# Kernel optimization log

Hardware: AMD Instinct MI355X
Metric: run time of the kernel (lower is better)

## Reference

```python
import jax, jax.numpy as jnp
import numpy as np

B, TT, TP, TO = 8, 128, 256, 512
V, D, H, L = 1024, 1024, 16, 12
FF = 4 * D
DH = D // H
EPS = 1e-5


def _pe(t, d):
    # sinusoidal PE: concat(sin(omega*t), cos(omega*t)), omega = exp(-ln(1e4)*i/(d/2))
    half = d // 2
    omega = jnp.exp(-jnp.log(10000.0) * jnp.arange(half, dtype=jnp.float32) / half)
    ang = jnp.arange(t, dtype=jnp.float32)[:, None] * omega[None, :]  # (t, d/2)
    return jnp.concatenate([jnp.sin(ang), jnp.cos(ang)], axis=-1)  # (t, d)


def _ln(x, g, b):
    mu = x.mean(axis=-1, keepdims=True)
    var = ((x - mu) ** 2).mean(axis=-1, keepdims=True)
    return (x - mu) / jnp.sqrt(var + EPS) * g + b


def _forward(text_ids, prompt_ids, output_ids, text_tab, prompt_tab, output_tab, sep,
             ln1_g, ln1_b, qkv_w, out_w, out_b, ln2_g, ln2_b,
             ff1_w, ff1_b, ff2_w, ff2_b, fc_w, fc_b):
    emb = lambda ids, tab: tab[ids] + _pe(ids.shape[1], D)[None]
    sep_tok = jnp.broadcast_to(sep, (B, 1, D))
    # join: [text, sep, prompt, sep, output]
    x = jnp.concatenate([emb(text_ids, text_tab), sep_tok,
                         emb(prompt_ids, prompt_tab), sep_tok,
                         emb(output_ids, output_tab)], axis=1)  # (B, T, D)
    T = x.shape[1]
    causal = jnp.tril(jnp.ones((T, T), dtype=bool))  # (T, T)
    scale = DH ** -0.5
    neg = -jnp.finfo(x.dtype).max
    for l in range(L):
        # attention block (prenorm residual); uniform lengths -> mask m is all ones
        h = _ln(x, ln1_g[l], ln1_b[l])
        qkv = h @ qkv_w[l]  # (B, T, 3D)
        q, k, v = jnp.split(qkv, 3, axis=-1)
        q = q.reshape(B, T, H, DH)
        k = k.reshape(B, T, H, DH)
        v = v.reshape(B, T, H, DH)
        e = jnp.einsum('bihd,bjhd->bijh', q, k) * scale
        e = jnp.where(causal[None, :, :, None], e, neg)
        a = jax.nn.softmax(e, axis=2)
        o = jnp.einsum('bijh,bjhd->bihd', a, v).reshape(B, T, D)
        x = x + o @ out_w[l] + out_b[l]
        # ffn block (prenorm residual), exact GELU as torch nn.GELU default
        h2 = _ln(x, ln2_g[l], ln2_b[l])
        ff = jax.nn.gelu(h2 @ ff1_w[l] + ff1_b[l], approximate=False) @ ff2_w[l] + ff2_b[l]
        x = x + ff
    h = x @ fc_w + fc_b  # (B, T, V)
    return h[:, -1, :]  # logits of last position, (B, V)


def setup_inputs() -> dict:
    key = jax.random.key(0)
    ks = iter(jax.random.split(key, 32))
    s = 0.02
    inp = {
        'text_ids': jax.random.randint(next(ks), (B, TT), 0, V),
        'prompt_ids': jax.random.randint(next(ks), (B, TP), 0, V),
        'output_ids': jax.random.randint(next(ks), (B, TO), 0, V),
        'text_tab': jax.random.normal(next(ks), (V, D), jnp.float32) * s,
        'prompt_tab': jax.random.normal(next(ks), (V, D), jnp.float32) * s,
        'output_tab': jax.random.normal(next(ks), (V, D), jnp.float32) * s,
        'sep': jax.random.normal(next(ks), (D,), jnp.float32),
        'ln1_g': jnp.ones((L, D), jnp.float32),
        'ln1_b': jnp.zeros((L, D), jnp.float32),
        'qkv_w': jax.random.normal(next(ks), (L, D, 3 * D), jnp.float32) * s,
        'out_w': jax.random.normal(next(ks), (L, D, D), jnp.float32) * s,
        'out_b': jnp.zeros((L, D), jnp.float32),
        'ln2_g': jnp.ones((L, D), jnp.float32),
        'ln2_b': jnp.zeros((L, D), jnp.float32),
        'ff1_w': jax.random.normal(next(ks), (L, D, FF), jnp.float32) * s,
        'ff1_b': jnp.zeros((L, FF), jnp.float32),
        'ff2_w': jax.random.normal(next(ks), (L, FF, D), jnp.float32) * s,
        'ff2_b': jnp.zeros((L, D), jnp.float32),
        'fc_w': jax.random.normal(next(ks), (D, V), jnp.float32) * s,
        'fc_b': jnp.zeros((V,), jnp.float32),
    }
    return inp


def reference(text_ids, prompt_ids, output_ids, text_tab, prompt_tab, output_tab, sep,
              ln1_g, ln1_b, qkv_w, out_w, out_b, ln2_g, ln2_b,
              ff1_w, ff1_b, ff2_w, ff2_b, fc_w, fc_b):
    return _forward(text_ids, prompt_ids, output_ids, text_tab, prompt_tab, output_tab, sep,
                    ln1_g, ln1_b, qkv_w, out_w, out_b, ln2_g, ln2_b,
                    ff1_w, ff1_b, ff2_w, ff2_b, fc_w, fc_b)
```

## Files before the change

### kernel.cpp

```cpp
#include <hip/hip_runtime.h>
#include <hip/hip_bf16.h>
#include <math.h>

#define Bn 8
#define Tn 898
#define Dn 1024
#define Hn 16
#define DHn 64
#define Ln 12
#define FFn 4096
#define Vn 1024
#define BT (Bn*Tn)

typedef short bf16x8 __attribute__((ext_vector_type(8)));
typedef float f32x4 __attribute__((ext_vector_type(4)));

__device__ __forceinline__ ushort f2bf(float f) {
    union { float f; unsigned u; } c; c.f = f;
    unsigned r = c.u + 0x7fffu + ((c.u >> 16) & 1u);
    return (ushort)(r >> 16);
}

__device__ __forceinline__ void glds16(const void* g, void* l) {
    __builtin_amdgcn_global_load_lds(
        (const __attribute__((address_space(1))) unsigned int*)g,
        (__attribute__((address_space(3))) unsigned int*)l, 16, 0, 0);
}

__global__ __launch_bounds__(256) void transpose_cast_kernel(
    const float* __restrict__ in, ushort* __restrict__ out,
    int K, int N, size_t in_ls, size_t out_ls)
{
    __shared__ ushort t[64][68];
    const float* inp = in + (size_t)blockIdx.z * in_ls;
    ushort* outp = out + (size_t)blockIdx.z * out_ls;
    int n0 = blockIdx.x * 64, k0 = blockIdx.y * 64;
    int tx = threadIdx.x & 63, ty = threadIdx.x >> 6;
    #pragma unroll
    for (int p = 0; p < 16; p++) {
        int kl = p * 4 + ty;
        t[tx][kl] = f2bf(inp[(size_t)(k0 + kl) * N + n0 + tx]);
    }
    __syncthreads();
    int tx4 = threadIdx.x & 15, ty4 = threadIdx.x >> 4;
    #pragma unroll
    for (int p = 0; p < 4; p++) {
        int nl = p * 16 + ty4;
        ushort4 v;
        v.x = t[nl][4*tx4]; v.y = t[nl][4*tx4+1]; v.z = t[nl][4*tx4+2]; v.w = t[nl][4*tx4+3];
        *(ushort4*)&outp[(size_t)(n0 + nl) * K + k0 + 4*tx4] = v;
    }
}

__global__ __launch_bounds__(256) void embed_kernel(
    const int* __restrict__ tids, const int* __restrict__ pids, const int* __restrict__ oids,
    const float* __restrict__ ttab, const float* __restrict__ ptab, const float* __restrict__ otab,
    const float* __restrict__ sep, float* __restrict__ x)
{
    int bp = blockIdx.x;
    int b = bp / Tn, pos = bp - b * Tn;
    int d0 = threadIdx.x * 4;
    float4 r;
    if (pos == 128 || pos == 385) {
        r = *(const float4*)(sep + d0);
    } else {
        int t; int id; const float* tab;
        if (pos < 128)      { t = pos;       id = tids[b*128 + t]; tab = ttab; }
        else if (pos < 385) { t = pos - 129; id = pids[b*256 + t]; tab = ptab; }
        else                { t = pos - 386; id = oids[b*512 + t]; tab = otab; }
        float4 e = *(const float4*)(tab + (size_t)id * Dn + d0);
        float pe[4];
        #pragma unroll
        for (int i = 0; i < 4; i++) {
            int d = d0 + i;
            int ii = d & 511;
            float omega = expf(-9.210340371976184f * (float)ii * (1.0f/512.0f));
            float ang = (float)t * omega;
            pe[i] = (d < 512) ? sinf(ang) : cosf(ang);
        }
        r.x = e.x + pe[0]; r.y = e.y + pe[1]; r.z = e.z + pe[2]; r.w = e.w + pe[3];
    }
    *(float4*)(x + (size_t)bp * Dn + d0) = r;
}

__global__ __launch_bounds__(256) void ln_kernel(
    const float* __restrict__ x, const float* __restrict__ g, const float* __restrict__ bt,
    ushort* __restrict__ out)
{
    __shared__ float red[8];
    int row = blockIdx.x, tid = threadIdx.x;
    float4 v = ((const float4*)(x + (size_t)row * Dn))[tid];
    float s = v.x + v.y + v.z + v.w;
    #pragma unroll
    for (int o = 32; o; o >>= 1) s += __shfl_down(s, o);
    if ((tid & 63) == 0) red[tid >> 6] = s;
    __syncthreads();
    float mu = (red[0] + red[1] + red[2] + red[3]) * (1.0f / Dn);
    float d0 = v.x - mu, d1 = v.y - mu, d2 = v.z - mu, d3 = v.w - mu;
    float s2 = d0*d0 + d1*d1 + d2*d2 + d3*d3;
    #pragma unroll
    for (int o = 32; o; o >>= 1) s2 += __shfl_down(s2, o);
    if ((tid & 63) == 0) red[4 + (tid >> 6)] = s2;
    __syncthreads();
    float var = (red[4] + red[5] + red[6] + red[7]) * (1.0f / Dn);
    float rstd = rsqrtf(var + 1e-5f);
    float4 gg = ((const float4*)g)[tid];
    float4 bb = ((const float4*)bt)[tid];
    ushort4 o4;
    o4.x = f2bf(d0 * rstd * gg.x + bb.x);
    o4.y = f2bf(d1 * rstd * gg.y + bb.y);
    o4.z = f2bf(d2 * rstd * gg.z + bb.z);
    o4.w = f2bf(d3 * rstd * gg.w + bb.w);
    ((ushort4*)(out + (size_t)row * Dn))[tid] = o4;
}

template<int MODE>
__global__ __launch_bounds__(256) void gemm_kernel(
    const ushort* __restrict__ A, const ushort* __restrict__ Bw,
    const float* __restrict__ bias, const float* __restrict__ resid,
    void* __restrict__ Cout, int M, int N, int K)
{
    __shared__ ushort Asm[128 * 32];
    __shared__ ushort Bsm[128 * 32];
    int tid = threadIdx.x;
    int lane = tid & 63, wv = tid >> 6;
    int wm = wv >> 1, wn = wv & 1;
    int m0 = blockIdx.y * 128, n0 = blockIdx.x * 128;
    int l16 = lane & 15, lhi = lane >> 4;

    f32x4 acc[4][4];
    #pragma unroll
    for (int i = 0; i < 4; i++)
        #pragma unroll
        for (int j = 0; j < 4; j++) acc[i][j] = (f32x4){0.f, 0.f, 0.f, 0.f};

    int srow = wv * 16 + (lane >> 2);
    int skc  = (lane & 3) * 8;
    const ushort* Ap0 = A  + (size_t)(m0 + srow) * K + skc;
    const ushort* Ap1 = A  + (size_t)(m0 + 64 + srow) * K + skc;
    const ushort* Bp0 = Bw + (size_t)(n0 + srow) * K + skc;
    const ushort* Bp1 = Bw + (size_t)(n0 + 64 + srow) * K + skc;
    ushort* ldsA0 = &Asm[wv * 512];
    ushort* ldsA1 = &Asm[2048 + wv * 512];
    ushort* ldsB0 = &Bsm[wv * 512];
    ushort* ldsB1 = &Bsm[2048 + wv * 512];

    for (int kk = 0; kk < K; kk += 32) {
        __syncthreads();
        glds16(Ap0 + kk, ldsA0);
        glds16(Ap1 + kk, ldsA1);
        glds16(Bp0 + kk, ldsB0);
        glds16(Bp1 + kk, ldsB1);
        __syncthreads();

        bf16x8 af[4], bfr[4];
        #pragma unroll
        for (int mi = 0; mi < 4; mi++)
            af[mi] = *(const bf16x8*)&Asm[(wm*64 + mi*16 + l16) * 32 + lhi*8];
        #pragma unroll
        for (int ni = 0; ni < 4; ni++)
            bfr[ni] = *(const bf16x8*)&Bsm[(wn*64 + ni*16 + l16) * 32 + lhi*8];
        #pragma unroll
        for (int mi = 0; mi < 4; mi++)
            #pragma unroll
            for (int ni = 0; ni < 4; ni++)
                acc[mi][ni] = __builtin_amdgcn_mfma_f32_16x16x32_bf16(af[mi], bfr[ni], acc[mi][ni], 0, 0, 0);
    }

    #pragma unroll
    for (int mi = 0; mi < 4; mi++) {
        int rl = wm*64 + mi*16 + lhi*4;
        #pragma unroll
        for (int ni = 0; ni < 4; ni++) {
            int gcol = n0 + wn*64 + ni*16 + l16;
            float bs = (MODE == 0) ? 0.0f : bias[gcol];
            #pragma unroll
            for (int j = 0; j < 4; j++) {
                int grow = m0 + rl + j;
                if (grow >= M) continue;
                float v = acc[mi][ni][j] + bs;
                if (MODE == 1) {
                    float r = resid[(size_t)grow * N + gcol];
                    ((float*)Cout)[(size_t)grow * N + gcol] = r + v;
                } else if (MODE == 2) {
                    v = 0.5f * v * (1.0f + erff(v * 0.70710678118654752f));
                    ((ushort*)Cout)[(size_t)grow * N + gcol] = f2bf(v);
                } else {
                    ((ushort*)Cout)[(size_t)grow * N + gcol] = f2bf(v);
                }
            }
        }
    }
}

__global__ __launch_bounds__(256) void attn_kernel(
    const ushort* __restrict__ qkv, ushort* __restrict__ out)
{
    __shared__ ushort Ksm[64 * 72];
    __shared__ ushort Vsm[64 * 72];
    __shared__ ushort Psm[4][16 * 72];
    int qt = blockIdx.x, b = blockIdx.y, h = blockIdx.z;
    int tid = threadIdx.x, lane = tid & 63, wave = tid >> 6;
    int l16 = lane & 15, lhi = lane >> 4;

    int qrow = qt*64 + wave*16 + l16;
    bf16x8 qf0 = {}, qf1 = {};
    if (qrow < Tn) {
        const ushort* qp = qkv + (size_t)(b*Tn + qrow) * 3072 + h*64 + lhi*8;
        qf0 = *(const bf16x8*)qp;
        qf1 = *(const bf16x8*)(qp + 32);
    }

    f32x4 o[4];
    #pragma unroll
    for (int i = 0; i < 4; i++) o[i] = (f32x4){0.f,0.f,0.f,0.f};
    float mrun[4] = {-1e30f,-1e30f,-1e30f,-1e30f};
    float sume[4] = {0.f,0.f,0.f,0.f};

    int kr = tid >> 2, cc = (tid & 3) * 16;
    const ushort* kvbase = qkv + (size_t)(b*Tn) * 3072 + h*64 + cc;
    int qg = qt*64 + wave*16 + lhi*4;

    for (int jt = 0; jt <= qt; jt++) {
        int kvr = jt*64 + kr;
        uint4 k0 = make_uint4(0,0,0,0), k1 = k0, v0 = k0, v1 = k0;
        if (kvr < Tn) {
            const ushort* p = kvbase + (size_t)kvr * 3072;
            k0 = *(const uint4*)(p + 1024);
            k1 = *(const uint4*)(p + 1024 + 8);
            v0 = *(const uint4*)(p + 2048);
            v1 = *(const uint4*)(p + 2048 + 8);
        }
        __syncthreads();
        *(uint4*)&Ksm[kr * 72 + cc] = k0;
        *(uint4*)&Ksm[kr * 72 + cc + 8] = k1;
        {
            ushort vv[16];
            *(uint4*)&vv[0] = v0; *(uint4*)&vv[8] = v1;
            #pragma unroll
            for (int i = 0; i < 16; i++) Vsm[(cc + i) * 72 + kr] = vv[i];
        }
        __syncthreads();

        f32x4 s[4];
        #pragma unroll
        for (int ni = 0; ni < 4; ni++) {
            s[ni] = (f32x4){0.f,0.f,0.f,0.f};
            bf16x8 kf0 = *(const bf16x8*)&Ksm[(ni*16 + l16) * 72 + lhi*8];
            bf16x8 kf1 = *(const bf16x8*)&Ksm[(ni*16 + l16) * 72 + lhi*8 + 32];
            s[ni] = __builtin_amdgcn_mfma_f32_16x16x32_bf16(qf0, kf0, s[ni], 0, 0, 0);
            s[ni] = __builtin_amdgcn_mfma_f32_16x16x32_bf16(qf1, kf1, s[ni], 0, 0, 0);
        }

        float pv[4][4];
        #pragma unroll
        for (int j = 0; j < 4; j++) {
            int qgj = qg + j;
            float mx = -1e30f;
            #pragma unroll
            for (int ni = 0; ni < 4; ni++) {
                int kvg = jt*64 + ni*16 + l16;
                float e = (kvg <= qgj && kvg < Tn) ? s[ni][j] * 0.125f : -1e30f;
                pv[ni][j] = e;
                mx = fmaxf(mx, e);
            }
            #pragma unroll
            for (int m = 1; m < 16; m <<= 1) mx = fmaxf(mx, __shfl_xor(mx, m));
            float mnew = fmaxf(mrun[j], mx);
            float fac = expf(mrun[j] - mnew);
            mrun[j] = mnew;
            float rs = 0.f;
            #pragma unroll
            for (int ni = 0; ni < 4; ni++) { pv[ni][j] = expf(pv[ni][j] - mnew); rs += pv[ni][j]; }
            #pragma unroll
            for (int m = 1; m < 16; m <<= 1) rs += __shfl_xor(rs, m);
            sume[j] = sume[j] * fac + rs;
            #pragma unroll
            for (int di = 0; di < 4; di++) o[di][j] *= fac;
        }

        #pragma unroll
        for (int j = 0; j < 4; j++)
            #pragma unroll
            for (int ni = 0; ni < 4; ni++)
                Psm[wave][(lhi*4 + j) * 72 + ni*16 + l16] = f2bf(pv[ni][j]);
        __syncthreads();

        bf16x8 pf0 = *(const bf16x8*)&Psm[wave][l16 * 72 + lhi*8];
        bf16x8 pf1 = *(const bf16x8*)&Psm[wave][l16 * 72 + lhi*8 + 32];
        #pragma unroll
        for (int di = 0; di < 4; di++) {
            bf16x8 vf0 = *(const bf16x8*)&Vsm[(di*16 + l16) * 72 + lhi*8];
            bf16x8 vf1 = *(const bf16x8*)&Vsm[(di*16 + l16) * 72 + lhi*8 + 32];
            o[di] = __builtin_amdgcn_mfma_f32_16x16x32_bf16(pf0, vf0, o[di], 0, 0, 0);
            o[di] = __builtin_amdgcn_mfma_f32_16x16x32_bf16(pf1, vf1, o[di], 0, 0, 0);
        }
    }

    #pragma unroll
    for (int j = 0; j < 4; j++) {
        int qgj = qg + j;
        if (qgj >= Tn) continue;
        float inv = 1.0f / sume[j];
        #pragma unroll
        for (int di = 0; di < 4; di++)
            out[(size_t)(b*Tn + qgj) * Dn + h*64 + di*16 + l16] = f2bf(o[di][j] * inv);
    }
}

__global__ __launch_bounds__(256) void fc_kernel(
    const float* __restrict__ x, const float* __restrict__ w,
    const float* __restrict__ bias, float* __restrict__ out)
{
    __shared__ float xs[Dn];
    int b = blockIdx.y;
    int v = blockIdx.x * 256 + threadIdx.x;
    float4 t = ((const float4*)(x + (size_t)(b*Tn + Tn - 1) * Dn))[threadIdx.x];
    ((float4*)xs)[threadIdx.x] = t;
    __syncthreads();
    float acc = bias[v];
    for (int d = 0; d < Dn; d++)
        acc = fmaf(xs[d], w[(size_t)d * Vn + v], acc);
    out[(size_t)b * Vn + v] = acc;
}

extern "C" void kernel_launch(void* const* d_in, const int* in_sizes, int n_in,
                              void* d_out, int out_size, void* d_ws, size_t ws_size,
                              hipStream_t stream)
{
    const int*   text_ids  = (const int*)d_in[0];
    const int*   prompt_ids= (const int*)d_in[1];
    const int*   output_ids= (const int*)d_in[2];
    const float* text_tab  = (const float*)d_in[3];
    const float* prompt_tab= (const float*)d_in[4];
    const float* output_tab= (const float*)d_in[5];
    const float* sep       = (const float*)d_in[6];
    const float* ln1_g     = (const float*)d_in[7];
    const float* ln1_b     = (const float*)d_in[8];
    const float* qkv_w     = (const float*)d_in[9];
    const float* out_w     = (const float*)d_in[10];
    const float* out_b     = (const float*)d_in[11];
    const float* ln2_g     = (const float*)d_in[12];
    const float* ln2_b     = (const float*)d_in[13];
    const float* ff1_w     = (const float*)d_in[14];
    const float* ff1_b     = (const float*)d_in[15];
    const float* ff2_w     = (const float*)d_in[16];
    const float* ff2_b     = (const float*)d_in[17];
    const float* fc_w      = (const float*)d_in[18];
    const float* fc_b      = (const float*)d_in[19];

    char* ws = (char*)d_ws;
    float*  x    = (float*)(ws);
    ushort* h    = (ushort*)(ws + 29425664);
    ushort* qkv  = (ushort*)(ws + 44138496);
    ushort* attn = (ushort*)(ws + 88276992);
    ushort* ff1o = (ushort*)(ws + 102989824);
    ushort* wT   = (ushort*)(ws + 161841152);

    const size_t L_STRIDE = 12582912;
    const size_t OFF_QKV = 0, OFF_OUT = 3145728, OFF_FF1 = 4194304, OFF_FF2 = 8388608;
    const size_t upfront_need = 161841152ULL + 2ULL * L_STRIDE * Ln;
    const bool upfront = ws_size >= upfront_need;
    const int ZL = upfront ? Ln : 1;

    if (upfront) {
        transpose_cast_kernel<<<dim3(48,16,Ln), 256, 0, stream>>>(qkv_w, wT + OFF_QKV, Dn, 3*Dn, (size_t)Dn*3*Dn, L_STRIDE);
        transpose_cast_kernel<<<dim3(16,16,Ln), 256, 0, stream>>>(out_w, wT + OFF_OUT, Dn, Dn,   (size_t)Dn*Dn,   L_STRIDE);
        transpose_cast_kernel<<<dim3(64,16,Ln), 256, 0, stream>>>(ff1_w, wT + OFF_FF1, Dn, FFn,  (size_t)Dn*FFn,  L_STRIDE);
        transpose_cast_kernel<<<dim3(16,64,Ln), 256, 0, stream>>>(ff2_w, wT + OFF_FF2, FFn, Dn,  (size_t)FFn*Dn,  L_STRIDE);
    }

    embed_kernel<<<BT, 256, 0, stream>>>(text_ids, prompt_ids, output_ids,
                                         text_tab, prompt_tab, output_tab, sep, x);

    const int MT = 57;
    for (int l = 0; l < Ln; l++) {
        ushort* wbase = upfront ? (wT + (size_t)l * L_STRIDE) : wT;
        if (!upfront) {
            transpose_cast_kernel<<<dim3(48,16,1), 256, 0, stream>>>(qkv_w + (size_t)l*Dn*3*Dn, wbase + OFF_QKV, Dn, 3*Dn, 0, 0);
            transpose_cast_kernel<<<dim3(16,16,1), 256, 0, stream>>>(out_w + (size_t)l*Dn*Dn,   wbase + OFF_OUT, Dn, Dn,   0, 0);
            transpose_cast_kernel<<<dim3(64,16,1), 256, 0, stream>>>(ff1_w + (size_t)l*Dn*FFn,  wbase + OFF_FF1, Dn, FFn,  0, 0);
            transpose_cast_kernel<<<dim3(16,64,1), 256, 0, stream>>>(ff2_w + (size_t)l*FFn*Dn,  wbase + OFF_FF2, FFn, Dn,  0, 0);
        }
        ln_kernel<<<BT, 256, 0, stream>>>(x, ln1_g + l*Dn, ln1_b + l*Dn, h);
        gemm_kernel<0><<<dim3(3*Dn/128, MT), 256, 0, stream>>>(
            h, wbase + OFF_QKV, nullptr, nullptr, qkv, BT, 3*Dn, Dn);
        attn_kernel<<<dim3(15, Bn, Hn), 256, 0, stream>>>(qkv, attn);
        gemm_kernel<1><<<dim3(Dn/128, MT), 256, 0, stream>>>(
            attn, wbase + OFF_OUT, out_b + l*Dn, x, x, BT, Dn, Dn);
        ln_kernel<<<BT, 256, 0, stream>>>(x, ln2_g + l*Dn, ln2_b + l*Dn, h);
        gemm_kernel<2><<<dim3(FFn/128, MT), 256, 0, stream>>>(
            h, wbase + OFF_FF1, ff1_b + l*FFn, nullptr, ff1o, BT, FFn, Dn);
        gemm_kernel<1><<<dim3(Dn/128, MT), 256, 0, stream>>>(
            ff1o, wbase + OFF_FF2, ff2_b + l*Dn, x, x, BT, Dn, FFn);
    }

    fc_kernel<<<dim3(Vn/256, Bn), 256, 0, stream>>>(x, fc_w, fc_b, (float*)d_out);
}
```

Before: 5.908 ms.

## Rewrite GEMM with templated tiles, double-buffered LDS, and XCD-aware block mapping

Replaces the fixed 128x128, K=32 GEMM with a templated kernel. The kernel double-buffers 64-wide K tiles in LDS, so loads for the next tile overlap the current tile's MFMAs, and it needs one barrier per step instead of two. QKV and FF1 use 256x256 tiles with 8 waves, while out-proj and FF2 keep 128x128. Blocks are remapped so contiguous tiles land on the same XCD to improve L2 reuse. Workspace offsets grow to cover the padded M of 29x256 rows, since A loads past row 7184 now read into the enlarged buffers.

```diff
diff --git a/kernel.cpp b/kernel.cpp
--- a/kernel.cpp
+++ b/kernel.cpp
@@ -11,6 +11,7 @@
 #define FFn 4096
 #define Vn 1024
 #define BT (Bn*Tn)
+#define MP 7424
 
 typedef short bf16x8 __attribute__((ext_vector_type(8)));
 typedef float f32x4 __attribute__((ext_vector_type(4)));
@@ -114,65 +115,91 @@
     ((ushort4*)(out + (size_t)row * Dn))[tid] = o4;
 }
 
-template<int MODE>
-__global__ __launch_bounds__(256) void gemm_kernel(
+template<int BM, int BN, int WM, int WN, int MODE>
+__global__ __launch_bounds__(WM*WN*64) void gemm2_kernel(
     const ushort* __restrict__ A, const ushort* __restrict__ Bw,
     const float* __restrict__ bias, const float* __restrict__ resid,
-    void* __restrict__ Cout, int M, int N, int K)
-{
-    __shared__ ushort Asm[128 * 32];
-    __shared__ ushort Bsm[128 * 32];
-    int tid = threadIdx.x;
-    int lane = tid & 63, wv = tid >> 6;
-    int wm = wv >> 1, wn = wv & 1;
-    int m0 = blockIdx.y * 128, n0 = blockIdx.x * 128;
+    void* __restrict__ Cout, int M, int N, int K, int nx)
+{
+    constexpr int NWAVE = WM * WN;
+    constexpr int MI = BM / WM / 16;
+    constexpr int NI = BN / WN / 16;
+    constexpr int GA = (BM / 8) / NWAVE;
+    constexpr int GB = (BN / 8) / NWAVE;
+
+    __shared__ ushort sA[2][BM * 64];
+    __shared__ ushort sB[2][BN * 64];
+
+    int tid = threadIdx.x, lane = tid & 63, wv = tid >> 6;
+    int wm = wv / WN, wn = wv % WN;
     int l16 = lane & 15, lhi = lane >> 4;
 
-    f32x4 acc[4][4];
-    #pragma unroll
-    for (int i = 0; i < 4; i++)
-        #pragma unroll
-        for (int j = 0; j < 4; j++) acc[i][j] = (f32x4){0.f, 0.f, 0.f, 0.f};
-
-    int srow = wv * 16 + (lane >> 2);
-    int skc  = (lane & 3) * 8;
-    const ushort* Ap0 = A  + (size_t)(m0 + srow) * K + skc;
-    const ushort* Ap1 = A  + (size_t)(m0 + 64 + srow) * K + skc;
-    const ushort* Bp0 = Bw + (size_t)(n0 + srow) * K + skc;
-    const ushort* Bp1 = Bw + (size_t)(n0 + 64 + srow) * K + skc;
-    ushort* ldsA0 = &Asm[wv * 512];
-    ushort* ldsA1 = &Asm[2048 + wv * 512];
-    ushort* ldsB0 = &Bsm[wv * 512];
-    ushort* ldsB1 = &Bsm[2048 + wv * 512];
-
-    for (int kk = 0; kk < K; kk += 32) {
+    int nb = gridDim.x, bid = blockIdx.x;
+    int q = nb >> 3, r = nb & 7;
+    int xcd = bid & 7, idx = bid >> 3;
+    int wg = (xcd < r ? xcd * (q + 1) : r * (q + 1) + (xcd - r) * q) + idx;
+    int mt = wg / nx, ntt = wg - mt * nx;
+    int m0 = mt * BM, n0 = ntt * BN;
+
+    f32x4 acc[MI][NI];
+    #pragma unroll
+    for (int i = 0; i < MI; i++)
+        #pragma unroll
+        for (int j = 0; j < NI; j++) acc[i][j] = (f32x4){0.f, 0.f, 0.f, 0.f};
+
+    const int sr = lane >> 3;
+    const int sc = (lane & 7) * 8;
+    const ushort* Ab = A + (size_t)m0 * K + sc;
+    const ushort* Bb = Bw + (size_t)n0 * K + sc;
+
+    auto STAGE = [&](int buf, int kk) {
+        #pragma unroll
+        for (int i = 0; i < GA; i++) {
+            int rg = wv * GA + i;
+            glds16(Ab + (size_t)(rg * 8 + sr) * K + kk, &sA[buf][rg * 512]);
+        }
+        #pragma unroll
+        for (int i = 0; i < GB; i++) {
+            int rg = wv * GB + i;
+            glds16(Bb + (size_t)(rg * 8 + sr) * K + kk, &sB[buf][rg * 512]);
+        }
+    };
+
+    auto COMPUTE = [&](int buf) {
+        #pragma unroll
+        for (int ks = 0; ks < 2; ks++) {
+            bf16x8 af[MI], bfr[NI];
+            #pragma unroll
+            for (int mi = 0; mi < MI; mi++)
+                af[mi] = *(const bf16x8*)&sA[buf][(wm * (16 * MI) + mi * 16 + l16) * 64 + ks * 32 + lhi * 8];
+            #pragma unroll
+            for (int ni = 0; ni < NI; ni++)
+                bfr[ni] = *(const bf16x8*)&sB[buf][(wn * (16 * NI) + ni * 16 + l16) * 64 + ks * 32 + lhi * 8];
+            #pragma unroll
+            for (int mi = 0; mi < MI; mi++)
+                #pragma unroll
+                for (int ni = 0; ni < NI; ni++)
+                    acc[mi][ni] = __builtin_amdgcn_mfma_f32_16x16x32_bf16(af[mi], bfr[ni], acc[mi][ni], 0, 0, 0);
+        }
+    };
+
+    int ntile = K >> 6;
+    STAGE(0, 0);
+    __syncthreads();
+    int cur = 0;
+    for (int t = 0; t < ntile; t++) {
+        if (t + 1 < ntile) STAGE(cur ^ 1, (t + 1) * 64);
+        COMPUTE(cur);
         __syncthreads();
-        glds16(Ap0 + kk, ldsA0);
-        glds16(Ap1 + kk, ldsA1);
-        glds16(Bp0 + kk, ldsB0);
-        glds16(Bp1 + kk, ldsB1);
-        __syncthreads();
-
-        bf16x8 af[4], bfr[4];
-        #pragma unroll
-        for (int mi = 0; mi < 4; mi++)
-            af[mi] = *(const bf16x8*)&Asm[(wm*64 + mi*16 + l16) * 32 + lhi*8];
-        #pragma unroll
-        for (int ni = 0; ni < 4; ni++)
-            bfr[ni] = *(const bf16x8*)&Bsm[(wn*64 + ni*16 + l16) * 32 + lhi*8];
-        #pragma unroll
-        for (int mi = 0; mi < 4; mi++)
-            #pragma unroll
-            for (int ni = 0; ni < 4; ni++)
-                acc[mi][ni] = __builtin_amdgcn_mfma_f32_16x16x32_bf16(af[mi], bfr[ni], acc[mi][ni], 0, 0, 0);
-    }
-
-    #pragma unroll
-    for (int mi = 0; mi < 4; mi++) {
-        int rl = wm*64 + mi*16 + lhi*4;
-        #pragma unroll
-        for (int ni = 0; ni < 4; ni++) {
-            int gcol = n0 + wn*64 + ni*16 + l16;
+        cur ^= 1;
+    }
+
+    #pragma unroll
+    for (int mi = 0; mi < MI; mi++) {
+        int rl = wm * (16 * MI) + mi * 16 + lhi * 4;
+        #pragma unroll
+        for (int ni = 0; ni < NI; ni++) {
+            int gcol = n0 + wn * (16 * NI) + ni * 16 + l16;
             float bs = (MODE == 0) ? 0.0f : bias[gcol];
             #pragma unroll
             for (int j = 0; j < 4; j++) {
@@ -180,8 +207,8 @@
                 if (grow >= M) continue;
                 float v = acc[mi][ni][j] + bs;
                 if (MODE == 1) {
-                    float r = resid[(size_t)grow * N + gcol];
-                    ((float*)Cout)[(size_t)grow * N + gcol] = r + v;
+                    float rr = resid[(size_t)grow * N + gcol];
+                    ((float*)Cout)[(size_t)grow * N + gcol] = rr + v;
                 } else if (MODE == 2) {
                     v = 0.5f * v * (1.0f + erff(v * 0.70710678118654752f));
                     ((ushort*)Cout)[(size_t)grow * N + gcol] = f2bf(v);
@@ -352,16 +379,15 @@
     char* ws = (char*)d_ws;
     float*  x    = (float*)(ws);
     ushort* h    = (ushort*)(ws + 29425664);
-    ushort* qkv  = (ushort*)(ws + 44138496);
-    ushort* attn = (ushort*)(ws + 88276992);
-    ushort* ff1o = (ushort*)(ws + 102989824);
-    ushort* wT   = (ushort*)(ws + 161841152);
+    ushort* qkv  = (ushort*)(ws + 44630016);
+    ushort* attn = (ushort*)(ws + 90243072);
+    ushort* ff1o = (ushort*)(ws + 105447424);
+    ushort* wT   = (ushort*)(ws + 166264832);
 
     const size_t L_STRIDE = 12582912;
     const size_t OFF_QKV = 0, OFF_OUT = 3145728, OFF_FF1 = 4194304, OFF_FF2 = 8388608;
-    const size_t upfront_need = 161841152ULL + 2ULL * L_STRIDE * Ln;
+    const size_t upfront_need = 166264832ULL + 2ULL * L_STRIDE * Ln;
     const bool upfront = ws_size >= upfront_need;
-    const int ZL = upfront ? Ln : 1;
 
     if (upfront) {
         transpose_cast_kernel<<<dim3(48,16,Ln), 256, 0, stream>>>(qkv_w, wT + OFF_QKV, Dn, 3*Dn, (size_t)Dn*3*Dn, L_STRIDE);
@@ -373,26 +399,25 @@
     embed_kernel<<<BT, 256, 0, stream>>>(text_ids, prompt_ids, output_ids,
                                          text_tab, prompt_tab, output_tab, sep, x);
 
-    const int MT = 57;
     for (int l = 0; l < Ln; l++) {
-        ushort* wbase = upfront ? (wT + (size_t)l * L_STRIDE) : wT;
+        ushort* wb = upfront ? (wT + (size_t)l * L_STRIDE) : wT;
         if (!upfront) {
-            transpose_cast_kernel<<<dim3(48,16,1), 256, 0, stream>>>(qkv_w + (size_t)l*Dn*3*Dn, wbase + OFF_QKV, Dn, 3*Dn, 0, 0);
-            transpose_cast_kernel<<<dim3(16,16,1), 256, 0, stream>>>(out_w + (size_t)l*Dn*Dn,   wbase + OFF_OUT, Dn, Dn,   0, 0);
-            transpose_cast_kernel<<<dim3(64,16,1), 256, 0, stream>>>(ff1_w + (size_t)l*Dn*FFn,  wbase + OFF_FF1, Dn, FFn,  0, 0);
-            transpose_cast_kernel<<<dim3(16,64,1), 256, 0, stream>>>(ff2_w + (size_t)l*FFn*Dn,  wbase + OFF_FF2, FFn, Dn,  0, 0);
+            transpose_cast_kernel<<<dim3(48,16,1), 256, 0, stream>>>(qkv_w + (size_t)l*Dn*3*Dn, wb + OFF_QKV, Dn, 3*Dn, 0, 0);
+            transpose_cast_kernel<<<dim3(16,16,1), 256, 0, stream>>>(out_w + (size_t)l*Dn*Dn,   wb + OFF_OUT, Dn, Dn,   0, 0);
+            transpose_cast_kernel<<<dim3(64,16,1), 256, 0, stream>>>(ff1_w + (size_t)l*Dn*FFn,  wb + OFF_FF1, Dn, FFn,  0, 0);
+            transpose_cast_kernel<<<dim3(16,64,1), 256, 0, stream>>>(ff2_w + (size_t)l*FFn*Dn,  wb + OFF_FF2, FFn, Dn,  0, 0);
         }
         ln_kernel<<<BT, 256, 0, stream>>>(x, ln1_g + l*Dn, ln1_b + l*Dn, h);
-        gemm_kernel<0><<<dim3(3*Dn/128, MT), 256, 0, stream>>>(
-            h, wbase + OFF_QKV, nullptr, nullptr, qkv, BT, 3*Dn, Dn);
+        gemm2_kernel<256,256,2,4,0><<<12*29, 512, 0, stream>>>(
+            h, wb + OFF_QKV, nullptr, nullptr, qkv, BT, 3*Dn, Dn, 12);
         attn_kernel<<<dim3(15, Bn, Hn), 256, 0, stream>>>(qkv, attn);
-        gemm_kernel<1><<<dim3(Dn/128, MT), 256, 0, stream>>>(
-            attn, wbase + OFF_OUT, out_b + l*Dn, x, x, BT, Dn, Dn);
+        gemm2_kernel<128,128,2,2,1><<<8*57, 256, 0, stream>>>(
+            attn, wb + OFF_OUT, out_b + l*Dn, x, x, BT, Dn, Dn, 8);
         ln_kernel<<<BT, 256, 0, stream>>>(x, ln2_g + l*Dn, ln2_b + l*Dn, h);
-        gemm_kernel<2><<<dim3(FFn/128, MT), 256, 0, stream>>>(
-            h, wbase + OFF_FF1, ff1_b + l*FFn, nullptr, ff1o, BT, FFn, Dn);
-        gemm_kernel<1><<<dim3(Dn/128, MT), 256, 0, stream>>>(
-            ff1o, wbase + OFF_FF2, ff2_b + l*Dn, x, x, BT, Dn, FFn);
+        gemm2_kernel<256,256,2,4,2><<<16*29, 512, 0, stream>>>(
+            h, wb + OFF_FF1, ff1_b + l*FFn, nullptr, ff1o, BT, FFn, Dn, 16);
+        gemm2_kernel<128,128,2,2,1><<<8*57, 256, 0, stream>>>(
+            ff1o, wb + OFF_FF2, ff2_b + l*Dn, x, x, BT, Dn, FFn, 8);
     }
 
     fc_kernel<<<dim3(Vn/256, Bn), 256, 0, stream>>>(x, fc_w, fc_b, (float*)d_out);
```

Result: slower. 6.158 ms (+4.2%).

## Triple-buffer GEMM LDS loads with swizzle and XCD-aware tile remapping

Applied to the files above, without the earlier changes.

Replaces the GEMM main loop with a 3-stage LDS pipeline. Global-to-LDS loads for tile t+2 are issued before computing tile t, and explicit vmcnt waits replace the double __syncthreads per iteration. LDS chunks are XOR-swizzled to reduce bank conflicts, and a 1D grid is remapped so each XCD gets a contiguous range of tiles for better L2 locality. Workspace offsets shift to leave padding. The cost is three times the LDS footprint, occupancy hinted at 3 blocks per CU, and reliance on exact hand-counted vmcnt values.

```diff
diff --git a/kernel.cpp b/kernel.cpp
--- a/kernel.cpp
+++ b/kernel.cpp
@@ -26,6 +26,10 @@
         (const __attribute__((address_space(1))) unsigned int*)g,
         (__attribute__((address_space(3))) unsigned int*)l, 16, 0, 0);
 }
+
+#define BARRIER() __builtin_amdgcn_s_barrier()
+#define VMCNT4() asm volatile("s_waitcnt vmcnt(4)" ::: "memory")
+#define VMCNT0() asm volatile("s_waitcnt vmcnt(0)" ::: "memory")
 
 __global__ __launch_bounds__(256) void transpose_cast_kernel(
     const float* __restrict__ in, ushort* __restrict__ out,
@@ -115,64 +119,89 @@
 }
 
 template<int MODE>
-__global__ __launch_bounds__(256) void gemm_kernel(
+__global__ __launch_bounds__(256, 3) void gemm3_kernel(
     const ushort* __restrict__ A, const ushort* __restrict__ Bw,
     const float* __restrict__ bias, const float* __restrict__ resid,
-    void* __restrict__ Cout, int M, int N, int K)
-{
-    __shared__ ushort Asm[128 * 32];
-    __shared__ ushort Bsm[128 * 32];
-    int tid = threadIdx.x;
-    int lane = tid & 63, wv = tid >> 6;
+    void* __restrict__ Cout, int M, int N, int K, int nx)
+{
+    __shared__ ushort sA[3][128 * 32];
+    __shared__ ushort sB[3][128 * 32];
+
+    int tid = threadIdx.x, lane = tid & 63, wv = tid >> 6;
     int wm = wv >> 1, wn = wv & 1;
-    int m0 = blockIdx.y * 128, n0 = blockIdx.x * 128;
     int l16 = lane & 15, lhi = lane >> 4;
 
+    int nb = gridDim.x, bid = blockIdx.x;
+    int qq = nb >> 3, rr8 = nb & 7;
+    int xcd = bid & 7, idx = bid >> 3;
+    int wg = (xcd < rr8 ? xcd * (qq + 1) : rr8 * (qq + 1) + (xcd - rr8) * qq) + idx;
+    int mt = wg / nx, ntt = wg - mt * nx;
+    int m0 = mt * 128, n0 = ntt * 128;
+
     f32x4 acc[4][4];
     #pragma unroll
     for (int i = 0; i < 4; i++)
         #pragma unroll
         for (int j = 0; j < 4; j++) acc[i][j] = (f32x4){0.f, 0.f, 0.f, 0.f};
 
-    int srow = wv * 16 + (lane >> 2);
-    int skc  = (lane & 3) * 8;
-    const ushort* Ap0 = A  + (size_t)(m0 + srow) * K + skc;
-    const ushort* Ap1 = A  + (size_t)(m0 + 64 + srow) * K + skc;
-    const ushort* Bp0 = Bw + (size_t)(n0 + srow) * K + skc;
-    const ushort* Bp1 = Bw + (size_t)(n0 + 64 + srow) * K + skc;
-    ushort* ldsA0 = &Asm[wv * 512];
-    ushort* ldsA1 = &Asm[2048 + wv * 512];
-    ushort* ldsB0 = &Bsm[wv * 512];
-    ushort* ldsB1 = &Bsm[2048 + wv * 512];
-
-    for (int kk = 0; kk < K; kk += 32) {
-        __syncthreads();
-        glds16(Ap0 + kk, ldsA0);
-        glds16(Ap1 + kk, ldsA1);
-        glds16(Bp0 + kk, ldsB0);
-        glds16(Bp1 + kk, ldsB1);
-        __syncthreads();
-
-        bf16x8 af[4], bfr[4];
+    const size_t K2 = (size_t)K * 2;
+    int srow = lane >> 2;
+    int schk = ((lane & 3) ^ (srow & 3)) * 16;
+    const char* Ab = (const char*)A + (size_t)(m0 + srow) * K2 + schk;
+    const char* Bb = (const char*)Bw + (size_t)(n0 + srow) * K2 + schk;
+    const int r0 = wv * 32, r1 = wv * 32 + 16;
+
+    auto stage = [&](int buf, int t) {
+        size_t ko = (size_t)t * 64;
+        glds16(Ab + (size_t)r0 * K2 + ko, (char*)&sA[buf][0] + r0 * 64);
+        glds16(Ab + (size_t)r1 * K2 + ko, (char*)&sA[buf][0] + r1 * 64);
+        glds16(Bb + (size_t)r0 * K2 + ko, (char*)&sB[buf][0] + r0 * 64);
+        glds16(Bb + (size_t)r1 * K2 + ko, (char*)&sB[buf][0] + r1 * 64);
+    };
+
+    const int sc = (lhi ^ (l16 & 3)) * 8;
+    auto compute = [&](int buf) {
+        bf16x8 af[4], bf[4];
         #pragma unroll
         for (int mi = 0; mi < 4; mi++)
-            af[mi] = *(const bf16x8*)&Asm[(wm*64 + mi*16 + l16) * 32 + lhi*8];
+            af[mi] = *(const bf16x8*)&sA[buf][(wm * 64 + mi * 16 + l16) * 32 + sc];
         #pragma unroll
         for (int ni = 0; ni < 4; ni++)
-            bfr[ni] = *(const bf16x8*)&Bsm[(wn*64 + ni*16 + l16) * 32 + lhi*8];
+            bf[ni] = *(const bf16x8*)&sB[buf][(wn * 64 + ni * 16 + l16) * 32 + sc];
         #pragma unroll
         for (int mi = 0; mi < 4; mi++)
             #pragma unroll
             for (int ni = 0; ni < 4; ni++)
-                acc[mi][ni] = __builtin_amdgcn_mfma_f32_16x16x32_bf16(af[mi], bfr[ni], acc[mi][ni], 0, 0, 0);
+                acc[mi][ni] = __builtin_amdgcn_mfma_f32_16x16x32_bf16(af[mi], bf[ni], acc[mi][ni], 0, 0, 0);
+    };
+
+    int ntile = K >> 5;
+    stage(0, 0);
+    stage(1, 1);
+    VMCNT4();
+    BARRIER();
+
+    int b = 0;
+    for (int t = 0; t < ntile; ++t) {
+        if (t + 2 < ntile) {
+            int pbuf = b + 2; if (pbuf >= 3) pbuf -= 3;
+            stage(pbuf, t + 2);
+            compute(b);
+            VMCNT4();
+        } else {
+            compute(b);
+            VMCNT0();
+        }
+        BARRIER();
+        if (++b == 3) b = 0;
     }
 
     #pragma unroll
     for (int mi = 0; mi < 4; mi++) {
-        int rl = wm*64 + mi*16 + lhi*4;
+        int rl = wm * 64 + mi * 16 + lhi * 4;
         #pragma unroll
         for (int ni = 0; ni < 4; ni++) {
-            int gcol = n0 + wn*64 + ni*16 + l16;
+            int gcol = n0 + wn * 64 + ni * 16 + l16;
             float bs = (MODE == 0) ? 0.0f : bias[gcol];
             #pragma unroll
             for (int j = 0; j < 4; j++) {
@@ -180,8 +209,8 @@
                 if (grow >= M) continue;
                 float v = acc[mi][ni][j] + bs;
                 if (MODE == 1) {
-                    float r = resid[(size_t)grow * N + gcol];
-                    ((float*)Cout)[(size_t)grow * N + gcol] = r + v;
+                    float rv = resid[(size_t)grow * N + gcol];
+                    ((float*)Cout)[(size_t)grow * N + gcol] = rv + v;
                 } else if (MODE == 2) {
                     v = 0.5f * v * (1.0f + erff(v * 0.70710678118654752f));
                     ((ushort*)Cout)[(size_t)grow * N + gcol] = f2bf(v);
@@ -352,16 +381,15 @@
     char* ws = (char*)d_ws;
     float*  x    = (float*)(ws);
     ushort* h    = (ushort*)(ws + 29425664);
-    ushort* qkv  = (ushort*)(ws + 44138496);
-    ushort* attn = (ushort*)(ws + 88276992);
-    ushort* ff1o = (ushort*)(ws + 102989824);
-    ushort* wT   = (ushort*)(ws + 161841152);
+    ushort* qkv  = (ushort*)(ws + 44630016);
+    ushort* attn = (ushort*)(ws + 90243072);
+    ushort* ff1o = (ushort*)(ws + 105447424);
+    ushort* wT   = (ushort*)(ws + 166264832);
 
     const size_t L_STRIDE = 12582912;
     const size_t OFF_QKV = 0, OFF_OUT = 3145728, OFF_FF1 = 4194304, OFF_FF2 = 8388608;
-    const size_t upfront_need = 161841152ULL + 2ULL * L_STRIDE * Ln;
+    const size_t upfront_need = 166264832ULL + 2ULL * L_STRIDE * Ln;
     const bool upfront = ws_size >= upfront_need;
-    const int ZL = upfront ? Ln : 1;
 
     if (upfront) {
         transpose_cast_kernel<<<dim3(48,16,Ln), 256, 0, stream>>>(qkv_w, wT + OFF_QKV, Dn, 3*Dn, (size_t)Dn*3*Dn, L_STRIDE);
@@ -373,26 +401,25 @@
     embed_kernel<<<BT, 256, 0, stream>>>(text_ids, prompt_ids, output_ids,
                                          text_tab, prompt_tab, output_tab, sep, x);
 
-    const int MT = 57;
     for (int l = 0; l < Ln; l++) {
-        ushort* wbase = upfront ? (wT + (size_t)l * L_STRIDE) : wT;
+        ushort* wb = upfront ? (wT + (size_t)l * L_STRIDE) : wT;
         if (!upfront) {
-            transpose_cast_kernel<<<dim3(48,16,1), 256, 0, stream>>>(qkv_w + (size_t)l*Dn*3*Dn, wbase + OFF_QKV, Dn, 3*Dn, 0, 0);
-            transpose_cast_kernel<<<dim3(16,16,1), 256, 0, stream>>>(out_w + (size_t)l*Dn*Dn,   wbase + OFF_OUT, Dn, Dn,   0, 0);
-            transpose_cast_kernel<<<dim3(64,16,1), 256, 0, stream>>>(ff1_w + (size_t)l*Dn*FFn,  wbase + OFF_FF1, Dn, FFn,  0, 0);
-            transpose_cast_kernel<<<dim3(16,64,1), 256, 0, stream>>>(ff2_w + (size_t)l*FFn*Dn,  wbase + OFF_FF2, FFn, Dn,  0, 0);
+            transpose_cast_kernel<<<dim3(48,16,1), 256, 0, stream>>>(qkv_w + (size_t)l*Dn*3*Dn, wb + OFF_QKV, Dn, 3*Dn, 0, 0);
+            transpose_cast_kernel<<<dim3(16,16,1), 256, 0, stream>>>(out_w + (size_t)l*Dn*Dn,   wb + OFF_OUT, Dn, Dn,   0, 0);
+            transpose_cast_kernel<<<dim3(64,16,1), 256, 0, stream>>>(ff1_w + (size_t)l*Dn*FFn,  wb + OFF_FF1, Dn, FFn,  0, 0);
+            transpose_cast_kernel<<<dim3(16,64,1), 256, 0, stream>>>(ff2_w + (size_t)l*FFn*Dn,  wb + OFF_FF2, FFn, Dn,  0, 0);
         }
         ln_kernel<<<BT, 256, 0, stream>>>(x, ln1_g + l*Dn, ln1_b + l*Dn, h);
-        gemm_kernel<0><<<dim3(3*Dn/128, MT), 256, 0, stream>>>(
-            h, wbase + OFF_QKV, nullptr, nullptr, qkv, BT, 3*Dn, Dn);
+        gemm3_kernel<0><<<57*24, 256, 0, stream>>>(
+            h, wb + OFF_QKV, nullptr, nullptr, qkv, BT, 3*Dn, Dn, 24);
         attn_kernel<<<dim3(15, Bn, Hn), 256, 0, stream>>>(qkv, attn);
-        gemm_kernel<1><<<dim3(Dn/128, MT), 256, 0, stream>>>(
-            attn, wbase + OFF_OUT, out_b + l*Dn, x, x, BT, Dn, Dn);
+        gemm3_kernel<1><<<57*8, 256, 0, stream>>>(
+            attn, wb + OFF_OUT, out_b + l*Dn, x, x, BT, Dn, Dn, 8);
         ln_kernel<<<BT, 256, 0, stream>>>(x, ln2_g + l*Dn, ln2_b + l*Dn, h);
-        gemm_kernel<2><<<dim3(FFn/128, MT), 256, 0, stream>>>(
-            h, wbase + OFF_FF1, ff1_b + l*FFn, nullptr, ff1o, BT, FFn, Dn);
-        gemm_kernel<1><<<dim3(Dn/128, MT), 256, 0, stream>>>(
-            ff1o, wbase + OFF_FF2, ff2_b + l*Dn, x, x, BT, Dn, FFn);
+        gemm3_kernel<2><<<57*32, 256, 0, stream>>>(
+            h, wb + OFF_FF1, ff1_b + l*FFn, nullptr, ff1o, BT, FFn, Dn, 32);
+        gemm3_kernel<1><<<57*8, 256, 0, stream>>>(
+            ff1o, wb + OFF_FF2, ff2_b + l*Dn, x, x, BT, Dn, FFn, 8);
     }
 
     fc_kernel<<<dim3(Vn/256, Bn), 256, 0, stream>>>(x, fc_w, fc_b, (float*)d_out);
```

Result: slower. 6.209 ms (+5.1%).
